# Optimization experiments

Measured on AMD Instinct MI355X. Metric: run time of the kernel, lower is better.

The kernel has to match this reference:

```python
import jax, jax.numpy as jnp
import numpy as np
from jax import lax

ALPHA = 1.5
N_ITER = 50  # entmax bisect default
GAIN = 1.414


def _p(z):
    # gp_inv(clamp(z,0), alpha) = z_+^(1/(alpha-1)) = z_+^2 for alpha=1.5
    zc = jnp.clip(z, 0.0, None)
    return zc * zc


def entmax15(X):
    """alpha-entmax (alpha=1.5) along last dim via bisection (entmax lib algorithm)."""
    d = X.shape[-1]
    Xs = X * (ALPHA - 1.0)
    mx = jnp.max(Xs, axis=-1, keepdims=True)
    tau_lo = mx - 1.0                       # gp(1, alpha) = 1
    tau_hi = mx - (1.0 / d) ** (ALPHA - 1.0)  # gp(1/d, alpha)
    f_lo = jnp.sum(_p(Xs - tau_lo), axis=-1, keepdims=True) - 1.0

    def body(i, carry):
        tau_lo, dm = carry
        dm = dm * 0.5
        tau_m = tau_lo + dm
        f_m = jnp.sum(_p(Xs - tau_m), axis=-1, keepdims=True) - 1.0
        tau_lo = jnp.where(f_m * f_lo >= 0.0, tau_m, tau_lo)
        return (tau_lo, dm)

    tau_lo, _ = lax.fori_loop(0, N_ITER, body, (tau_lo, tau_hi - tau_lo))
    p = _p(Xs - tau_lo)
    return p / jnp.sum(p, axis=-1, keepdims=True)  # ensure_sum_one=True


def _xavier(key, shape):
    std = GAIN * (2.0 / (shape[0] + shape[1])) ** 0.5
    a = (3.0 ** 0.5) * std
    return jax.random.uniform(key, shape, minval=-a, maxval=a, dtype=jnp.float32)


def setup_inputs() -> dict:
    B, F, E, N = 2048, 64, 256, 64  # batch, nfield, nemb, ncross
    key = jax.random.key(0)
    k1, k2, k3, k4 = jax.random.split(key, 4)
    return {
        "x": jax.random.normal(k1, (B, F, E), dtype=jnp.float32),
        "bilinear_w": _xavier(k2, (E, E)),
        "query": _xavier(k3, (N, E)),
        "value": _xavier(k4, (N, F)),
    }


def reference(x, bilinear_w, query, value):
    # x: [B,F,E]; bilinear_w: [E,E]; query: [N,E]; value: [N,F]
    scale = x.shape[-1] ** -0.5
    k = jnp.einsum('bfe,de->bfd', x, bilinear_w)        # [B,F,E]
    att_gate = jnp.einsum('bfd,nd->bnf', k, query) * scale  # [B,N,F]
    sparse_gate = entmax15(att_gate)                     # entmax over F
    attn_weight = sparse_gate * value[None]              # [B,N,F]
    return jnp.exp(jnp.einsum('bfe,bnf->bne', x, attn_weight))  # [B,N,E]
```

## Files before the change

### kernel.cpp

```cpp
#include <hip/hip_runtime.h>
#include <hip/hip_bf16.h>

typedef __attribute__((ext_vector_type(8))) short bf16x8;
typedef __attribute__((ext_vector_type(4))) float f32x4;

__device__ __forceinline__ unsigned int pk2(float a, float b) {
  union { __hip_bfloat162 h; unsigned int u; } cv;
  cv.h = __float22bfloat162_rn(make_float2(a, b));
  return cv.u;
}
__device__ __forceinline__ unsigned short f2bf(float f) {
  unsigned int u = __float_as_uint(f);
  u += 0x7FFFu + ((u >> 16) & 1u);
  return (unsigned short)(u >> 16);
}

__global__ void __launch_bounds__(256) qw_kernel(const float* __restrict__ q,
                                                 const float* __restrict__ W,
                                                 unsigned short* __restrict__ qw) {
  int n = blockIdx.x, e = threadIdx.x;
  float acc = 0.f;
  #pragma unroll 8
  for (int d = 0; d < 256; ++d) acc = fmaf(q[n * 256 + d], W[d * 256 + e], acc);
  qw[n * 256 + e] = f2bf(acc * 0.0625f);
}

__global__ void __launch_bounds__(512, 6) cross_main(
    const float* __restrict__ x, const float* __restrict__ value,
    const unsigned short* __restrict__ qw, float* __restrict__ out) {

  __shared__ __align__(16) unsigned short lds_x[64 * 268];
  __shared__ __align__(16) unsigned char  lds_pool[64 * 68 * 4];

  float* lds_att = (float*)lds_pool;
  unsigned short* lds_aw = (unsigned short*)lds_pool;

  const int t = threadIdx.x;
  const int b = blockIdx.x;
  const int l = t & 63;
  const int w = t >> 6;
  const int l15 = l & 15, l4 = l >> 4;

  {
    const float4* xg = (const float4*)(x + (size_t)b * 16384);
    #pragma unroll
    for (int it = 0; it < 4; ++it) {
      int u = it * 512 + t;
      float4 v0 = xg[2 * u], v1 = xg[2 * u + 1];
      int f = u >> 5, c8 = u & 31;
      char* dst = (char*)lds_x + f * 536 + c8 * 16;
      *(uint2*)dst       = make_uint2(pk2(v0.x, v0.y), pk2(v0.z, v0.w));
      *(uint2*)(dst + 8) = make_uint2(pk2(v1.x, v1.y), pk2(v1.z, v1.w));
    }
  }
  __syncthreads();

  {
    int nt = w >> 1, ft0 = (w & 1) * 2;
    f32x4 acc0 = {0.f, 0.f, 0.f, 0.f}, acc1 = {0.f, 0.f, 0.f, 0.f};
    const unsigned short* qa = qw + (nt * 16 + l15) * 256 + l4 * 8;
    const char* rb0 = (const char*)lds_x + (ft0 * 16 + l15) * 536 + l4 * 16;
    const char* rb1 = rb0 + 16 * 536;
    #pragma unroll
    for (int kc = 0; kc < 8; ++kc) {
      union BF { uint2 d[2]; bf16x8 v; };
      bf16x8 a = *(const bf16x8*)(qa + kc * 32);
      BF b0, b1;
      b0.d[0] = *(const uint2*)(rb0 + kc * 64);
      b0.d[1] = *(const uint2*)(rb0 + kc * 64 + 8);
      b1.d[0] = *(const uint2*)(rb1 + kc * 64);
      b1.d[1] = *(const uint2*)(rb1 + kc * 64 + 8);
      acc0 = __builtin_amdgcn_mfma_f32_16x16x32_bf16(a, b0.v, acc0, 0, 0, 0);
      acc1 = __builtin_amdgcn_mfma_f32_16x16x32_bf16(a, b1.v, acc1, 0, 0, 0);
    }
    int nrow = nt * 16 + 4 * l4;
    #pragma unroll
    for (int r = 0; r < 4; ++r) {
      lds_att[(nrow + r) * 68 + ft0 * 16 + l15]       = acc0[r];
      lds_att[(nrow + r) * 68 + (ft0 + 1) * 16 + l15] = acc1[r];
    }
  }
  __syncthreads();

  {
    int n = w * 8 + (l >> 3);
    int fb = (l & 7) * 8;
    f32x4 z0 = *(const f32x4*)&lds_att[n * 68 + fb];
    f32x4 z1 = *(const f32x4*)&lds_att[n * 68 + fb + 4];
    __syncthreads();
    float z[8];
    #pragma unroll
    for (int k = 0; k < 4; ++k) { z[k] = z0[k] * 0.5f; z[k + 4] = z1[k] * 0.5f; }
    float m = fmaxf(fmaxf(fmaxf(z[0], z[1]), fmaxf(z[2], z[3])),
                    fmaxf(fmaxf(z[4], z[5]), fmaxf(z[6], z[7])));
    m = fmaxf(m, __shfl_xor(m, 1));
    m = fmaxf(m, __shfl_xor(m, 2));
    m = fmaxf(m, __shfl_xor(m, 4));
    float tau = m - 1.0f;
    #pragma unroll
    for (int it = 0; it < 12; ++it) {
      float s0 = 0.f, s1 = 0.f, q0 = 0.f, q1 = 0.f;
      #pragma unroll
      for (int k = 0; k < 4; ++k) {
        float d0 = fmaxf(z[k] - tau, 0.f);
        float d1 = fmaxf(z[k + 4] - tau, 0.f);
        s0 = fmaf(d0, d0, s0); q0 += d0;
        s1 = fmaf(d1, d1, s1); q1 += d1;
      }
      float s = s0 + s1, q = q0 + q1;
      s += __shfl_xor(s, 1); s += __shfl_xor(s, 2); s += __shfl_xor(s, 4);
      q += __shfl_xor(q, 1); q += __shfl_xor(q, 2); q += __shfl_xor(q, 4);
      tau += (s - 1.0f) * 0.5f * __builtin_amdgcn_rcpf(q);
    }
    float p[8]; float S = 0.f;
    #pragma unroll
    for (int k = 0; k < 8; ++k) { float d = fmaxf(z[k] - tau, 0.f); p[k] = d * d; S += p[k]; }
    S += __shfl_xor(S, 1); S += __shfl_xor(S, 2); S += __shfl_xor(S, 4);
    float invS = 1.0f / S;
    const float4* vg = (const float4*)(value + n * 64 + fb);
    float4 va = vg[0], vb = vg[1];
    uint4 pkv;
    pkv.x = pk2(p[0] * invS * va.x, p[1] * invS * va.y);
    pkv.y = pk2(p[2] * invS * va.z, p[3] * invS * va.w);
    pkv.z = pk2(p[4] * invS * vb.x, p[5] * invS * vb.y);
    pkv.w = pk2(p[6] * invS * vb.z, p[7] * invS * vb.w);
    *(uint4*)&lds_aw[n * 72 + fb] = pkv;
  }
  __syncthreads();

  {
    const int te0 = 2 * w;
    f32x4 acc[4][2];
    #pragma unroll
    for (int nt = 0; nt < 4; ++nt) {
      acc[nt][0] = (f32x4){0.f, 0.f, 0.f, 0.f};
      acc[nt][1] = (f32x4){0.f, 0.f, 0.f, 0.f};
    }
    #pragma unroll
    for (int kc = 0; kc < 2; ++kc) {
      bf16x8 a[4];
      #pragma unroll
      for (int nt = 0; nt < 4; ++nt)
        a[nt] = *(const bf16x8*)&lds_aw[(nt * 16 + l15) * 72 + kc * 32 + l4 * 8];
      const char* gp = (const char*)lds_x + (kc * 32 + l4 * 8) * 536 + (te0 * 16 + l15) * 2;
      #pragma unroll
      for (int j = 0; j < 2; ++j) {
        union { unsigned short u[8]; bf16x8 v; } bb;
        #pragma unroll
        for (int i = 0; i < 8; ++i)
          bb.u[i] = *(const unsigned short*)(gp + i * 536 + j * 32);
        #pragma unroll
        for (int nt = 0; nt < 4; ++nt)
          acc[nt][j] = __builtin_amdgcn_mfma_f32_16x16x32_bf16(a[nt], bb.v, acc[nt][j], 0, 0, 0);
      }
    }
    float* ob = out + (size_t)b * 16384;
    #pragma unroll
    for (int nt = 0; nt < 4; ++nt) {
      #pragma unroll
      for (int j = 0; j < 2; ++j) {
        #pragma unroll
        for (int r = 0; r < 4; ++r) {
          ob[(nt * 16 + 4 * l4 + r) * 256 + (te0 + j) * 16 + l15] = __expf(acc[nt][j][r]);
        }
      }
    }
  }
}

extern "C" void kernel_launch(void* const* d_in, const int* in_sizes, int n_in,
                              void* d_out, int out_size, void* d_ws, size_t ws_size,
                              hipStream_t stream) {
  const float* x     = (const float*)d_in[0];
  const float* W     = (const float*)d_in[1];
  const float* q     = (const float*)d_in[2];
  const float* value = (const float*)d_in[3];
  float* out = (float*)d_out;
  unsigned short* qw = (unsigned short*)d_ws;

  qw_kernel<<<dim3(64), dim3(256), 0, stream>>>(q, W, qw);
  cross_main<<<dim3(2048), dim3(512), 0, stream>>>(x, value, qw, out);
}
```

Before: 71.52 us.

## Process two batches per block and prefetch second batch during first

Each block now handles two batch items (b and b+1024), halving the grid. Half of the second item's x tile is loaded into registers before the first item's compute, so its global latency overlaps with the GEMMs and entmax. This cuts block count and launch overhead but adds register pressure, which could reduce occupancy under launch_bounds(512,6), and halves the number of blocks available to hide latency.

```diff
diff --git a/kernel.cpp b/kernel.cpp
--- a/kernel.cpp
+++ b/kernel.cpp
@@ -36,26 +36,18 @@
   unsigned short* lds_aw = (unsigned short*)lds_pool;
 
   const int t = threadIdx.x;
-  const int b = blockIdx.x;
   const int l = t & 63;
   const int w = t >> 6;
   const int l15 = l & 15, l4 = l >> 4;
 
-  {
-    const float4* xg = (const float4*)(x + (size_t)b * 16384);
-    #pragma unroll
-    for (int it = 0; it < 4; ++it) {
-      int u = it * 512 + t;
-      float4 v0 = xg[2 * u], v1 = xg[2 * u + 1];
-      int f = u >> 5, c8 = u & 31;
-      char* dst = (char*)lds_x + f * 536 + c8 * 16;
-      *(uint2*)dst       = make_uint2(pk2(v0.x, v0.y), pk2(v0.z, v0.w));
-      *(uint2*)(dst + 8) = make_uint2(pk2(v1.x, v1.y), pk2(v1.z, v1.w));
-    }
-  }
-  __syncthreads();
-
-  {
+  auto stage_unit = [&](int u, float4 v0, float4 v1) {
+    int f = u >> 5, c8 = u & 31;
+    char* dst = (char*)lds_x + f * 536 + c8 * 16;
+    *(uint2*)dst       = make_uint2(pk2(v0.x, v0.y), pk2(v0.z, v0.w));
+    *(uint2*)(dst + 8) = make_uint2(pk2(v1.x, v1.y), pk2(v1.z, v1.w));
+  };
+
+  auto gemm1 = [&]() {
     int nt = w >> 1, ft0 = (w & 1) * 2;
     f32x4 acc0 = {0.f, 0.f, 0.f, 0.f}, acc1 = {0.f, 0.f, 0.f, 0.f};
     const unsigned short* qa = qw + (nt * 16 + l15) * 256 + l4 * 8;
@@ -79,10 +71,9 @@
       lds_att[(nrow + r) * 68 + ft0 * 16 + l15]       = acc0[r];
       lds_att[(nrow + r) * 68 + (ft0 + 1) * 16 + l15] = acc1[r];
     }
-  }
-  __syncthreads();
-
-  {
+  };
+
+  auto entmax_phase = [&]() {
     int n = w * 8 + (l >> 3);
     int fb = (l & 7) * 8;
     f32x4 z0 = *(const f32x4*)&lds_att[n * 68 + fb];
@@ -125,10 +116,9 @@
     pkv.z = pk2(p[4] * invS * vb.x, p[5] * invS * vb.y);
     pkv.w = pk2(p[6] * invS * vb.z, p[7] * invS * vb.w);
     *(uint4*)&lds_aw[n * 72 + fb] = pkv;
-  }
-  __syncthreads();
-
-  {
+  };
+
+  auto gemm2_store = [&](float* ob) {
     const int te0 = 2 * w;
     f32x4 acc[4][2];
     #pragma unroll
@@ -154,18 +144,48 @@
           acc[nt][j] = __builtin_amdgcn_mfma_f32_16x16x32_bf16(a[nt], bb.v, acc[nt][j], 0, 0, 0);
       }
     }
-    float* ob = out + (size_t)b * 16384;
-    #pragma unroll
-    for (int nt = 0; nt < 4; ++nt) {
-      #pragma unroll
-      for (int j = 0; j < 2; ++j) {
+    #pragma unroll
+    for (int nt = 0; nt < 4; ++nt)
+      #pragma unroll
+      for (int j = 0; j < 2; ++j)
         #pragma unroll
-        for (int r = 0; r < 4; ++r) {
+        for (int r = 0; r < 4; ++r)
           ob[(nt * 16 + 4 * l4 + r) * 256 + (te0 + j) * 16 + l15] = __expf(acc[nt][j][r]);
-        }
-      }
-    }
+  };
+
+  const size_t b0 = blockIdx.x, b1 = blockIdx.x + 1024;
+  const float4* xg0 = (const float4*)(x + b0 * 16384);
+  #pragma unroll
+  for (int it = 0; it < 4; ++it) {
+    int u = it * 512 + t;
+    stage_unit(u, xg0[2 * u], xg0[2 * u + 1]);
   }
+  const float4* xg1 = (const float4*)(x + b1 * 16384);
+  float4 pre0 = xg1[2 * t], pre1 = xg1[2 * t + 1];
+  float4 pre2 = xg1[2 * (512 + t)], pre3 = xg1[2 * (512 + t) + 1];
+  __syncthreads();
+
+  gemm1();
+  __syncthreads();
+  entmax_phase();
+  __syncthreads();
+  gemm2_store(out + b0 * 16384);
+  __syncthreads();
+
+  stage_unit(t, pre0, pre1);
+  stage_unit(512 + t, pre2, pre3);
+  #pragma unroll
+  for (int it = 2; it < 4; ++it) {
+    int u = it * 512 + t;
+    stage_unit(u, xg1[2 * u], xg1[2 * u + 1]);
+  }
+  __syncthreads();
+
+  gemm1();
+  __syncthreads();
+  entmax_phase();
+  __syncthreads();
+  gemm2_store(out + b1 * 16384);
 }
 
 extern "C" void kernel_launch(void* const* d_in, const int* in_sizes, int n_in,
@@ -179,5 +199,5 @@
   unsigned short* qw = (unsigned short*)d_ws;
 
   qw_kernel<<<dim3(64), dim3(256), 0, stream>>>(q, W, qw);
-  cross_main<<<dim3(2048), dim3(512), 0, stream>>>(x, value, qw, out);
-}
+  cross_main<<<dim3(1024), dim3(512), 0, stream>>>(x, value, qw, out);
+}
```

Result: slower. 104.0 us (+45.4%).

## Keep attention scores in registers and run entmax without LDS staging

Applied to the files above, without the earlier changes.

The score GEMM now swaps its MFMA operands so each wave produces a full 16×64 n-by-f tile. Each lane holds 16 scores for one n, so the entmax Newton iterations and normalisation run straight from registers using cross-lane shuffles over l4. This removes the fp32 score buffer in LDS and two block barriers. In exchange, waves 4–7 redundantly repeat the work of waves 0–3 and write the same lds_aw values. Global loads of x are also all issued up front before the bf16 conversion, to expose more memory-level parallelism.

```diff
diff --git a/kernel.cpp b/kernel.cpp
--- a/kernel.cpp
+++ b/kernel.cpp
@@ -30,101 +30,98 @@
     const unsigned short* __restrict__ qw, float* __restrict__ out) {
 
   __shared__ __align__(16) unsigned short lds_x[64 * 268];
-  __shared__ __align__(16) unsigned char  lds_pool[64 * 68 * 4];
-
-  float* lds_att = (float*)lds_pool;
-  unsigned short* lds_aw = (unsigned short*)lds_pool;
+  __shared__ __align__(16) unsigned short lds_aw[64 * 72];
 
   const int t = threadIdx.x;
   const int b = blockIdx.x;
   const int l = t & 63;
   const int w = t >> 6;
   const int l15 = l & 15, l4 = l >> 4;
+  const int nt = w & 3;
 
   {
     const float4* xg = (const float4*)(x + (size_t)b * 16384);
+    float4 v[8];
+    #pragma unroll
+    for (int it = 0; it < 4; ++it) {
+      v[2 * it]     = xg[2 * (it * 512 + t)];
+      v[2 * it + 1] = xg[2 * (it * 512 + t) + 1];
+    }
     #pragma unroll
     for (int it = 0; it < 4; ++it) {
       int u = it * 512 + t;
-      float4 v0 = xg[2 * u], v1 = xg[2 * u + 1];
       int f = u >> 5, c8 = u & 31;
       char* dst = (char*)lds_x + f * 536 + c8 * 16;
-      *(uint2*)dst       = make_uint2(pk2(v0.x, v0.y), pk2(v0.z, v0.w));
-      *(uint2*)(dst + 8) = make_uint2(pk2(v1.x, v1.y), pk2(v1.z, v1.w));
+      *(uint2*)dst       = make_uint2(pk2(v[2*it].x, v[2*it].y), pk2(v[2*it].z, v[2*it].w));
+      *(uint2*)(dst + 8) = make_uint2(pk2(v[2*it+1].x, v[2*it+1].y), pk2(v[2*it+1].z, v[2*it+1].w));
     }
   }
   __syncthreads();
 
+  f32x4 zz[4];
   {
-    int nt = w >> 1, ft0 = (w & 1) * 2;
-    f32x4 acc0 = {0.f, 0.f, 0.f, 0.f}, acc1 = {0.f, 0.f, 0.f, 0.f};
-    const unsigned short* qa = qw + (nt * 16 + l15) * 256 + l4 * 8;
-    const char* rb0 = (const char*)lds_x + (ft0 * 16 + l15) * 536 + l4 * 16;
-    const char* rb1 = rb0 + 16 * 536;
+    #pragma unroll
+    for (int tt = 0; tt < 4; ++tt) zz[tt] = (f32x4){0.f, 0.f, 0.f, 0.f};
+    const unsigned short* qb = qw + (nt * 16 + l15) * 256 + l4 * 8;
+    const char* xa = (const char*)lds_x + l15 * 536 + l4 * 16;
     #pragma unroll
     for (int kc = 0; kc < 8; ++kc) {
-      union BF { uint2 d[2]; bf16x8 v; };
-      bf16x8 a = *(const bf16x8*)(qa + kc * 32);
-      BF b0, b1;
-      b0.d[0] = *(const uint2*)(rb0 + kc * 64);
-      b0.d[1] = *(const uint2*)(rb0 + kc * 64 + 8);
-      b1.d[0] = *(const uint2*)(rb1 + kc * 64);
-      b1.d[1] = *(const uint2*)(rb1 + kc * 64 + 8);
-      acc0 = __builtin_amdgcn_mfma_f32_16x16x32_bf16(a, b0.v, acc0, 0, 0, 0);
-      acc1 = __builtin_amdgcn_mfma_f32_16x16x32_bf16(a, b1.v, acc1, 0, 0, 0);
-    }
-    int nrow = nt * 16 + 4 * l4;
-    #pragma unroll
-    for (int r = 0; r < 4; ++r) {
-      lds_att[(nrow + r) * 68 + ft0 * 16 + l15]       = acc0[r];
-      lds_att[(nrow + r) * 68 + (ft0 + 1) * 16 + l15] = acc1[r];
+      bf16x8 bq = *(const bf16x8*)(qb + kc * 32);
+      #pragma unroll
+      for (int tt = 0; tt < 4; ++tt) {
+        union BF { uint2 d[2]; bf16x8 v; } af;
+        const char* p = xa + tt * (16 * 536) + kc * 64;
+        af.d[0] = *(const uint2*)p;
+        af.d[1] = *(const uint2*)(p + 8);
+        zz[tt] = __builtin_amdgcn_mfma_f32_16x16x32_bf16(af.v, bq, zz[tt], 0, 0, 0);
+      }
     }
   }
-  __syncthreads();
 
   {
-    int n = w * 8 + (l >> 3);
-    int fb = (l & 7) * 8;
-    f32x4 z0 = *(const f32x4*)&lds_att[n * 68 + fb];
-    f32x4 z1 = *(const f32x4*)&lds_att[n * 68 + fb + 4];
-    __syncthreads();
-    float z[8];
+    const int n = nt * 16 + l15;
+    float z[16];
     #pragma unroll
-    for (int k = 0; k < 4; ++k) { z[k] = z0[k] * 0.5f; z[k + 4] = z1[k] * 0.5f; }
-    float m = fmaxf(fmaxf(fmaxf(z[0], z[1]), fmaxf(z[2], z[3])),
-                    fmaxf(fmaxf(z[4], z[5]), fmaxf(z[6], z[7])));
-    m = fmaxf(m, __shfl_xor(m, 1));
-    m = fmaxf(m, __shfl_xor(m, 2));
-    m = fmaxf(m, __shfl_xor(m, 4));
+    for (int tt = 0; tt < 4; ++tt)
+      #pragma unroll
+      for (int r = 0; r < 4; ++r) z[tt * 4 + r] = zz[tt][r] * 0.5f;
+
+    float m = z[0];
+    #pragma unroll
+    for (int k = 1; k < 16; ++k) m = fmaxf(m, z[k]);
+    m = fmaxf(m, __shfl_xor(m, 16));
+    m = fmaxf(m, __shfl_xor(m, 32));
+
     float tau = m - 1.0f;
     #pragma unroll
     for (int it = 0; it < 12; ++it) {
       float s0 = 0.f, s1 = 0.f, q0 = 0.f, q1 = 0.f;
       #pragma unroll
-      for (int k = 0; k < 4; ++k) {
+      for (int k = 0; k < 8; ++k) {
         float d0 = fmaxf(z[k] - tau, 0.f);
-        float d1 = fmaxf(z[k + 4] - tau, 0.f);
+        float d1 = fmaxf(z[k + 8] - tau, 0.f);
         s0 = fmaf(d0, d0, s0); q0 += d0;
         s1 = fmaf(d1, d1, s1); q1 += d1;
       }
       float s = s0 + s1, q = q0 + q1;
-      s += __shfl_xor(s, 1); s += __shfl_xor(s, 2); s += __shfl_xor(s, 4);
-      q += __shfl_xor(q, 1); q += __shfl_xor(q, 2); q += __shfl_xor(q, 4);
+      s += __shfl_xor(s, 16); s += __shfl_xor(s, 32);
+      q += __shfl_xor(q, 16); q += __shfl_xor(q, 32);
       tau += (s - 1.0f) * 0.5f * __builtin_amdgcn_rcpf(q);
     }
-    float p[8]; float S = 0.f;
+
+    float p[16]; float S = 0.f;
     #pragma unroll
-    for (int k = 0; k < 8; ++k) { float d = fmaxf(z[k] - tau, 0.f); p[k] = d * d; S += p[k]; }
-    S += __shfl_xor(S, 1); S += __shfl_xor(S, 2); S += __shfl_xor(S, 4);
+    for (int k = 0; k < 16; ++k) { float d = fmaxf(z[k] - tau, 0.f); p[k] = d * d; S += p[k]; }
+    S += __shfl_xor(S, 16); S += __shfl_xor(S, 32);
     float invS = 1.0f / S;
-    const float4* vg = (const float4*)(value + n * 64 + fb);
-    float4 va = vg[0], vb = vg[1];
-    uint4 pkv;
-    pkv.x = pk2(p[0] * invS * va.x, p[1] * invS * va.y);
-    pkv.y = pk2(p[2] * invS * va.z, p[3] * invS * va.w);
-    pkv.z = pk2(p[4] * invS * vb.x, p[5] * invS * vb.y);
-    pkv.w = pk2(p[6] * invS * vb.z, p[7] * invS * vb.w);
-    *(uint4*)&lds_aw[n * 72 + fb] = pkv;
+
+    #pragma unroll
+    for (int tt = 0; tt < 4; ++tt) {
+      float4 vv = *(const float4*)(value + n * 64 + tt * 16 + l4 * 4);
+      uint2 pkd = make_uint2(pk2(p[tt*4] * invS * vv.x,   p[tt*4+1] * invS * vv.y),
+                             pk2(p[tt*4+2] * invS * vv.z, p[tt*4+3] * invS * vv.w));
+      *(uint2*)&lds_aw[n * 72 + tt * 16 + l4 * 4] = pkd;
+    }
   }
   __syncthreads();
 
@@ -132,16 +129,16 @@
     const int te0 = 2 * w;
     f32x4 acc[4][2];
     #pragma unroll
-    for (int nt = 0; nt < 4; ++nt) {
-      acc[nt][0] = (f32x4){0.f, 0.f, 0.f, 0.f};
-      acc[nt][1] = (f32x4){0.f, 0.f, 0.f, 0.f};
+    for (int nt2 = 0; nt2 < 4; ++nt2) {
+      acc[nt2][0] = (f32x4){0.f, 0.f, 0.f, 0.f};
+      acc[nt2][1] = (f32x4){0.f, 0.f, 0.f, 0.f};
     }
     #pragma unroll
     for (int kc = 0; kc < 2; ++kc) {
       bf16x8 a[4];
       #pragma unroll
-      for (int nt = 0; nt < 4; ++nt)
-        a[nt] = *(const bf16x8*)&lds_aw[(nt * 16 + l15) * 72 + kc * 32 + l4 * 8];
+      for (int nt2 = 0; nt2 < 4; ++nt2)
+        a[nt2] = *(const bf16x8*)&lds_aw[(nt2 * 16 + l15) * 72 + kc * 32 + l4 * 8];
       const char* gp = (const char*)lds_x + (kc * 32 + l4 * 8) * 536 + (te0 * 16 + l15) * 2;
       #pragma unroll
       for (int j = 0; j < 2; ++j) {
@@ -150,21 +147,18 @@
         for (int i = 0; i < 8; ++i)
           bb.u[i] = *(const unsigned short*)(gp + i * 536 + j * 32);
         #pragma unroll
-        for (int nt = 0; nt < 4; ++nt)
-          acc[nt][j] = __builtin_amdgcn_mfma_f32_16x16x32_bf16(a[nt], bb.v, acc[nt][j], 0, 0, 0);
+        for (int nt2 = 0; nt2 < 4; ++nt2)
+          acc[nt2][j] = __builtin_amdgcn_mfma_f32_16x16x32_bf16(a[nt2], bb.v, acc[nt2][j], 0, 0, 0);
       }
     }
     float* ob = out + (size_t)b * 16384;
     #pragma unroll
-    for (int nt = 0; nt < 4; ++nt) {
+    for (int nt2 = 0; nt2 < 4; ++nt2)
       #pragma unroll
-      for (int j = 0; j < 2; ++j) {
+      for (int j = 0; j < 2; ++j)
         #pragma unroll
-        for (int r = 0; r < 4; ++r) {
-          ob[(nt * 16 + 4 * l4 + r) * 256 + (te0 + j) * 16 + l15] = __expf(acc[nt][j][r]);
-        }
-      }
-    }
+        for (int r = 0; r < 4; ++r)
+          ob[(nt2 * 16 + 4 * l4 + r) * 256 + (te0 + j) * 16 + l15] = __expf(acc[nt2][j][r]);
   }
 }
 
```

New measurement: 77.45 us. +8.3%, slower.

## Make blocks persistent over four batches with register prefetch of next x tile

Applied to the files above, without the earlier changes.

Each block now processes four consecutive batch elements in a loop. It prefetches the next batch's x tile into registers while computing the current one, hoists the value loads out of the loop, and reloads the qw fragments into registers once per iteration. Barriers become explicit lgkmcnt waits plus s_barrier, so outstanding global loads no longer stall at a barrier. The aim is to hide HBM load latency and amortise setup cost. In exchange the grid shrinks to 512 blocks, with fewer waves per CU (launch bounds 4), higher register pressure and possible tail imbalance.

```diff
diff --git a/kernel.cpp b/kernel.cpp
--- a/kernel.cpp
+++ b/kernel.cpp
@@ -13,6 +13,11 @@
   unsigned int u = __float_as_uint(f);
   u += 0x7FFFu + ((u >> 16) & 1u);
   return (unsigned short)(u >> 16);
+}
+
+__device__ __forceinline__ void lgkm_barrier() {
+  asm volatile("s_waitcnt lgkmcnt(0)" ::: "memory");
+  __builtin_amdgcn_s_barrier();
 }
 
 __global__ void __launch_bounds__(256) qw_kernel(const float* __restrict__ q,
@@ -25,7 +30,7 @@
   qw[n * 256 + e] = f2bf(acc * 0.0625f);
 }
 
-__global__ void __launch_bounds__(512, 6) cross_main(
+__global__ void __launch_bounds__(512, 4) cross_main(
     const float* __restrict__ x, const float* __restrict__ value,
     const unsigned short* __restrict__ qw, float* __restrict__ out) {
 
@@ -36,135 +41,157 @@
   unsigned short* lds_aw = (unsigned short*)lds_pool;
 
   const int t = threadIdx.x;
-  const int b = blockIdx.x;
   const int l = t & 63;
   const int w = t >> 6;
   const int l15 = l & 15, l4 = l >> 4;
 
+  float4 pre[8];
   {
-    const float4* xg = (const float4*)(x + (size_t)b * 16384);
+    const float4* xg = (const float4*)(x + (size_t)(4 * blockIdx.x) * 16384);
+    #pragma unroll
+    for (int it = 0; it < 4; ++it) {
+      pre[2 * it]     = xg[2 * (it * 512 + t)];
+      pre[2 * it + 1] = xg[2 * (it * 512 + t) + 1];
+    }
+  }
+  const int n_ent = w * 8 + (l >> 3);
+  const int fb_ent = (l & 7) * 8;
+  const float4 va = *(const float4*)(value + n_ent * 64 + fb_ent);
+  const float4 vb = *(const float4*)(value + n_ent * 64 + fb_ent + 4);
+
+  #pragma unroll 1
+  for (int bi = 0; bi < 4; ++bi) {
+    const size_t b = 4 * blockIdx.x + bi;
+
     #pragma unroll
     for (int it = 0; it < 4; ++it) {
       int u = it * 512 + t;
-      float4 v0 = xg[2 * u], v1 = xg[2 * u + 1];
       int f = u >> 5, c8 = u & 31;
       char* dst = (char*)lds_x + f * 536 + c8 * 16;
-      *(uint2*)dst       = make_uint2(pk2(v0.x, v0.y), pk2(v0.z, v0.w));
-      *(uint2*)(dst + 8) = make_uint2(pk2(v1.x, v1.y), pk2(v1.z, v1.w));
-    }
-  }
-  __syncthreads();
-
-  {
-    int nt = w >> 1, ft0 = (w & 1) * 2;
-    f32x4 acc0 = {0.f, 0.f, 0.f, 0.f}, acc1 = {0.f, 0.f, 0.f, 0.f};
-    const unsigned short* qa = qw + (nt * 16 + l15) * 256 + l4 * 8;
-    const char* rb0 = (const char*)lds_x + (ft0 * 16 + l15) * 536 + l4 * 16;
-    const char* rb1 = rb0 + 16 * 536;
-    #pragma unroll
-    for (int kc = 0; kc < 8; ++kc) {
-      union BF { uint2 d[2]; bf16x8 v; };
-      bf16x8 a = *(const bf16x8*)(qa + kc * 32);
-      BF b0, b1;
-      b0.d[0] = *(const uint2*)(rb0 + kc * 64);
-      b0.d[1] = *(const uint2*)(rb0 + kc * 64 + 8);
-      b1.d[0] = *(const uint2*)(rb1 + kc * 64);
-      b1.d[1] = *(const uint2*)(rb1 + kc * 64 + 8);
-      acc0 = __builtin_amdgcn_mfma_f32_16x16x32_bf16(a, b0.v, acc0, 0, 0, 0);
-      acc1 = __builtin_amdgcn_mfma_f32_16x16x32_bf16(a, b1.v, acc1, 0, 0, 0);
-    }
-    int nrow = nt * 16 + 4 * l4;
-    #pragma unroll
-    for (int r = 0; r < 4; ++r) {
-      lds_att[(nrow + r) * 68 + ft0 * 16 + l15]       = acc0[r];
-      lds_att[(nrow + r) * 68 + (ft0 + 1) * 16 + l15] = acc1[r];
-    }
-  }
-  __syncthreads();
-
-  {
-    int n = w * 8 + (l >> 3);
-    int fb = (l & 7) * 8;
-    f32x4 z0 = *(const f32x4*)&lds_att[n * 68 + fb];
-    f32x4 z1 = *(const f32x4*)&lds_att[n * 68 + fb + 4];
-    __syncthreads();
-    float z[8];
-    #pragma unroll
-    for (int k = 0; k < 4; ++k) { z[k] = z0[k] * 0.5f; z[k + 4] = z1[k] * 0.5f; }
-    float m = fmaxf(fmaxf(fmaxf(z[0], z[1]), fmaxf(z[2], z[3])),
-                    fmaxf(fmaxf(z[4], z[5]), fmaxf(z[6], z[7])));
-    m = fmaxf(m, __shfl_xor(m, 1));
-    m = fmaxf(m, __shfl_xor(m, 2));
-    m = fmaxf(m, __shfl_xor(m, 4));
-    float tau = m - 1.0f;
-    #pragma unroll
-    for (int it = 0; it < 12; ++it) {
-      float s0 = 0.f, s1 = 0.f, q0 = 0.f, q1 = 0.f;
-      #pragma unroll
-      for (int k = 0; k < 4; ++k) {
-        float d0 = fmaxf(z[k] - tau, 0.f);
-        float d1 = fmaxf(z[k + 4] - tau, 0.f);
-        s0 = fmaf(d0, d0, s0); q0 += d0;
-        s1 = fmaf(d1, d1, s1); q1 += d1;
-      }
-      float s = s0 + s1, q = q0 + q1;
-      s += __shfl_xor(s, 1); s += __shfl_xor(s, 2); s += __shfl_xor(s, 4);
-      q += __shfl_xor(q, 1); q += __shfl_xor(q, 2); q += __shfl_xor(q, 4);
-      tau += (s - 1.0f) * 0.5f * __builtin_amdgcn_rcpf(q);
-    }
-    float p[8]; float S = 0.f;
-    #pragma unroll
-    for (int k = 0; k < 8; ++k) { float d = fmaxf(z[k] - tau, 0.f); p[k] = d * d; S += p[k]; }
-    S += __shfl_xor(S, 1); S += __shfl_xor(S, 2); S += __shfl_xor(S, 4);
-    float invS = 1.0f / S;
-    const float4* vg = (const float4*)(value + n * 64 + fb);
-    float4 va = vg[0], vb = vg[1];
-    uint4 pkv;
-    pkv.x = pk2(p[0] * invS * va.x, p[1] * invS * va.y);
-    pkv.y = pk2(p[2] * invS * va.z, p[3] * invS * va.w);
-    pkv.z = pk2(p[4] * invS * vb.x, p[5] * invS * vb.y);
-    pkv.w = pk2(p[6] * invS * vb.z, p[7] * invS * vb.w);
-    *(uint4*)&lds_aw[n * 72 + fb] = pkv;
-  }
-  __syncthreads();
-
-  {
-    const int te0 = 2 * w;
-    f32x4 acc[4][2];
-    #pragma unroll
-    for (int nt = 0; nt < 4; ++nt) {
-      acc[nt][0] = (f32x4){0.f, 0.f, 0.f, 0.f};
-      acc[nt][1] = (f32x4){0.f, 0.f, 0.f, 0.f};
-    }
-    #pragma unroll
-    for (int kc = 0; kc < 2; ++kc) {
-      bf16x8 a[4];
-      #pragma unroll
-      for (int nt = 0; nt < 4; ++nt)
-        a[nt] = *(const bf16x8*)&lds_aw[(nt * 16 + l15) * 72 + kc * 32 + l4 * 8];
-      const char* gp = (const char*)lds_x + (kc * 32 + l4 * 8) * 536 + (te0 * 16 + l15) * 2;
-      #pragma unroll
-      for (int j = 0; j < 2; ++j) {
-        union { unsigned short u[8]; bf16x8 v; } bb;
-        #pragma unroll
-        for (int i = 0; i < 8; ++i)
-          bb.u[i] = *(const unsigned short*)(gp + i * 536 + j * 32);
-        #pragma unroll
-        for (int nt = 0; nt < 4; ++nt)
-          acc[nt][j] = __builtin_amdgcn_mfma_f32_16x16x32_bf16(a[nt], bb.v, acc[nt][j], 0, 0, 0);
-      }
-    }
-    float* ob = out + (size_t)b * 16384;
-    #pragma unroll
-    for (int nt = 0; nt < 4; ++nt) {
-      #pragma unroll
-      for (int j = 0; j < 2; ++j) {
-        #pragma unroll
-        for (int r = 0; r < 4; ++r) {
-          ob[(nt * 16 + 4 * l4 + r) * 256 + (te0 + j) * 16 + l15] = __expf(acc[nt][j][r]);
+      *(uint2*)dst       = make_uint2(pk2(pre[2*it].x, pre[2*it].y), pk2(pre[2*it].z, pre[2*it].w));
+      *(uint2*)(dst + 8) = make_uint2(pk2(pre[2*it+1].x, pre[2*it+1].y), pk2(pre[2*it+1].z, pre[2*it+1].w));
+    }
+
+    const int nt = w >> 1, ft0 = (w & 1) * 2;
+    bf16x8 qf[8];
+    {
+      const unsigned short* qa = qw + (nt * 16 + l15) * 256 + l4 * 8;
+      #pragma unroll
+      for (int kc = 0; kc < 8; ++kc) qf[kc] = *(const bf16x8*)(qa + kc * 32);
+    }
+    if (bi < 3) {
+      const float4* xg1 = (const float4*)(x + (b + 1) * 16384);
+      #pragma unroll
+      for (int it = 0; it < 4; ++it) {
+        pre[2 * it]     = xg1[2 * (it * 512 + t)];
+        pre[2 * it + 1] = xg1[2 * (it * 512 + t) + 1];
+      }
+    }
+    __builtin_amdgcn_sched_barrier(0);
+    lgkm_barrier();
+
+    {
+      f32x4 acc0 = {0.f, 0.f, 0.f, 0.f}, acc1 = {0.f, 0.f, 0.f, 0.f};
+      const char* rb0 = (const char*)lds_x + (ft0 * 16 + l15) * 536 + l4 * 16;
+      const char* rb1 = rb0 + 16 * 536;
+      #pragma unroll
+      for (int kc = 0; kc < 8; ++kc) {
+        union BF { uint2 d[2]; bf16x8 v; };
+        BF b0, b1;
+        b0.d[0] = *(const uint2*)(rb0 + kc * 64);
+        b0.d[1] = *(const uint2*)(rb0 + kc * 64 + 8);
+        b1.d[0] = *(const uint2*)(rb1 + kc * 64);
+        b1.d[1] = *(const uint2*)(rb1 + kc * 64 + 8);
+        acc0 = __builtin_amdgcn_mfma_f32_16x16x32_bf16(qf[kc], b0.v, acc0, 0, 0, 0);
+        acc1 = __builtin_amdgcn_mfma_f32_16x16x32_bf16(qf[kc], b1.v, acc1, 0, 0, 0);
+      }
+      int nrow = nt * 16 + 4 * l4;
+      #pragma unroll
+      for (int r = 0; r < 4; ++r) {
+        lds_att[(nrow + r) * 68 + ft0 * 16 + l15]       = acc0[r];
+        lds_att[(nrow + r) * 68 + (ft0 + 1) * 16 + l15] = acc1[r];
+      }
+    }
+    lgkm_barrier();
+
+    {
+      f32x4 z0 = *(const f32x4*)&lds_att[n_ent * 68 + fb_ent];
+      f32x4 z1 = *(const f32x4*)&lds_att[n_ent * 68 + fb_ent + 4];
+      lgkm_barrier();
+      float z[8];
+      #pragma unroll
+      for (int k = 0; k < 4; ++k) { z[k] = z0[k] * 0.5f; z[k + 4] = z1[k] * 0.5f; }
+      float m = fmaxf(fmaxf(fmaxf(z[0], z[1]), fmaxf(z[2], z[3])),
+                      fmaxf(fmaxf(z[4], z[5]), fmaxf(z[6], z[7])));
+      m = fmaxf(m, __shfl_xor(m, 1));
+      m = fmaxf(m, __shfl_xor(m, 2));
+      m = fmaxf(m, __shfl_xor(m, 4));
+      float tau = m - 1.0f;
+      #pragma unroll
+      for (int it = 0; it < 12; ++it) {
+        float s0 = 0.f, s1 = 0.f, q0 = 0.f, q1 = 0.f;
+        #pragma unroll
+        for (int k = 0; k < 4; ++k) {
+          float d0 = fmaxf(z[k] - tau, 0.f);
+          float d1 = fmaxf(z[k + 4] - tau, 0.f);
+          s0 = fmaf(d0, d0, s0); q0 += d0;
+          s1 = fmaf(d1, d1, s1); q1 += d1;
         }
-      }
-    }
+        float s = s0 + s1, q = q0 + q1;
+        s += __shfl_xor(s, 1); s += __shfl_xor(s, 2); s += __shfl_xor(s, 4);
+        q += __shfl_xor(q, 1); q += __shfl_xor(q, 2); q += __shfl_xor(q, 4);
+        tau += (s - 1.0f) * 0.5f * __builtin_amdgcn_rcpf(q);
+      }
+      float p[8]; float S = 0.f;
+      #pragma unroll
+      for (int k = 0; k < 8; ++k) { float d = fmaxf(z[k] - tau, 0.f); p[k] = d * d; S += p[k]; }
+      S += __shfl_xor(S, 1); S += __shfl_xor(S, 2); S += __shfl_xor(S, 4);
+      float invS = 1.0f / S;
+      uint4 pkv;
+      pkv.x = pk2(p[0] * invS * va.x, p[1] * invS * va.y);
+      pkv.y = pk2(p[2] * invS * va.z, p[3] * invS * va.w);
+      pkv.z = pk2(p[4] * invS * vb.x, p[5] * invS * vb.y);
+      pkv.w = pk2(p[6] * invS * vb.z, p[7] * invS * vb.w);
+      *(uint4*)&lds_aw[n_ent * 72 + fb_ent] = pkv;
+    }
+    lgkm_barrier();
+
+    {
+      const int te0 = 2 * w;
+      f32x4 acc[4][2];
+      #pragma unroll
+      for (int nt2 = 0; nt2 < 4; ++nt2) {
+        acc[nt2][0] = (f32x4){0.f, 0.f, 0.f, 0.f};
+        acc[nt2][1] = (f32x4){0.f, 0.f, 0.f, 0.f};
+      }
+      #pragma unroll
+      for (int kc = 0; kc < 2; ++kc) {
+        bf16x8 a[4];
+        #pragma unroll
+        for (int nt2 = 0; nt2 < 4; ++nt2)
+          a[nt2] = *(const bf16x8*)&lds_aw[(nt2 * 16 + l15) * 72 + kc * 32 + l4 * 8];
+        const char* gp = (const char*)lds_x + (kc * 32 + l4 * 8) * 536 + (te0 * 16 + l15) * 2;
+        #pragma unroll
+        for (int j = 0; j < 2; ++j) {
+          union { unsigned short u[8]; bf16x8 v; } bb;
+          #pragma unroll
+          for (int i = 0; i < 8; ++i)
+            bb.u[i] = *(const unsigned short*)(gp + i * 536 + j * 32);
+          #pragma unroll
+          for (int nt2 = 0; nt2 < 4; ++nt2)
+            acc[nt2][j] = __builtin_amdgcn_mfma_f32_16x16x32_bf16(a[nt2], bb.v, acc[nt2][j], 0, 0, 0);
+        }
+      }
+      float* ob = out + b * 16384;
+      #pragma unroll
+      for (int nt2 = 0; nt2 < 4; ++nt2)
+        #pragma unroll
+        for (int j = 0; j < 2; ++j)
+          #pragma unroll
+          for (int r = 0; r < 4; ++r)
+            ob[(nt2 * 16 + 4 * l4 + r) * 256 + (te0 + j) * 16 + l15] = __expf(acc[nt2][j][r]);
+    }
+    lgkm_barrier();
   }
 }
 
@@ -179,5 +206,5 @@
   unsigned short* qw = (unsigned short*)d_ws;
 
   qw_kernel<<<dim3(64), dim3(256), 0, stream>>>(q, W, qw);
-  cross_main<<<dim3(2048), dim3(512), 0, stream>>>(x, value, qw, out);
-}
+  cross_main<<<dim3(512), dim3(512), 0, stream>>>(x, value, qw, out);
+}
```

Result: slower. 137.7 us (+92.5%).
